# Optimization experiments

Measured on AMD Instinct MI355X. Metric: run time of the kernel, lower is better.

Reference implementation:

```python
import jax, jax.numpy as jnp
import numpy as np

N, C, HW, HEADS = 2048, 16, 8, 4
F = C * HW * HW  # 1024
E = 16384
EPS = 1e-5
NEG_SLOPE = 0.2


def _bn(x, g, b):
    # training-mode BatchNorm2d over (N, H, W)
    m = x.mean(axis=(0, 2, 3), keepdims=True)
    v = x.var(axis=(0, 2, 3), keepdims=True)
    return (x - m) * jax.lax.rsqrt(v + EPS) * g[None, :, None, None] + b[None, :, None, None]


def _conv1x1(x, w, b):
    # 1x1 conv == per-pixel linear: w is [out_c, in_c]
    return jnp.einsum('nchw,oc->nohw', x, w) + b[None, :, None, None]


def _gatv2(xf, edge_index, wl, bl, wr, br, att, bias_gat):
    # xf: [N, F] node features
    xl = (xf @ wl + bl).reshape(N, HEADS, F)  # source-side transform (lin_l)
    xr = (xf @ wr + br).reshape(N, HEADS, F)  # target-side transform (lin_r)
    src, dst = edge_index[0], edge_index[1]
    loops = jnp.arange(N)
    # PyG default: remove existing self loops (mask them) then add self loops
    src_f = jnp.concatenate([src, loops])
    dst_f = jnp.concatenate([dst, loops])
    valid = jnp.concatenate([src != dst, jnp.ones((N,), bool)])
    xj = xl[src_f]                                   # [E+N, HEADS, F] gather
    e = jax.nn.leaky_relu(xj + xr[dst_f], negative_slope=NEG_SLOPE)
    logits = jnp.einsum('ehf,hf->eh', e, att)        # [E+N, HEADS]
    logits = jnp.where(valid[:, None], logits, -jnp.inf)
    mx = jax.lax.stop_gradient(jax.ops.segment_max(logits, dst_f, num_segments=N))
    expv = jnp.where(valid[:, None], jnp.exp(logits - mx[dst_f]), 0.0)
    denom = jax.ops.segment_sum(expv, dst_f, num_segments=N)
    alpha = expv / denom[dst_f]                      # segment softmax over incoming edges
    out = jax.ops.segment_sum(alpha[:, :, None] * xj, dst_f, num_segments=N)  # [N, HEADS, F]
    return out.reshape(N, HEADS * F) + bias_gat


def setup_inputs() -> dict:
    key = jax.random.key(0)
    ks = jax.random.split(key, 8)
    s = 0.02
    return {
        'x': jax.random.normal(ks[0], (N, C, HW, HW), jnp.float32),
        'edge_index': jax.random.randint(ks[1], (2, E), 0, N),
        'w1': jax.random.normal(ks[2], (C, C), jnp.float32) * s,
        'b1': jnp.zeros((C,), jnp.float32),
        'g1': jnp.ones((C,), jnp.float32),
        'be1': jnp.zeros((C,), jnp.float32),
        'wl': jax.random.normal(ks[3], (F, HEADS * F), jnp.float32) * s,
        'bl': jnp.zeros((HEADS * F,), jnp.float32),
        'wr': jax.random.normal(ks[4], (F, HEADS * F), jnp.float32) * s,
        'br': jnp.zeros((HEADS * F,), jnp.float32),
        'att': jax.random.normal(ks[5], (HEADS, F), jnp.float32) * s,
        'bias_gat': jnp.zeros((HEADS * F,), jnp.float32),
        'w2': jax.random.normal(ks[6], (C, HEADS * C), jnp.float32) * s,
        'b2': jnp.zeros((C,), jnp.float32),
        'g2': jnp.ones((C,), jnp.float32),
        'be2': jnp.zeros((C,), jnp.float32),
    }


def reference(x, edge_index, w1, b1, g1, be1, wl, bl, wr, br, att, bias_gat, w2, b2, g2, be2):
    res = x
    y = _bn(_conv1x1(x, w1, b1), g1, be1)            # fc1: Conv2d 1x1 + BN
    yf = y.reshape(N, F)
    g = _gatv2(yf, edge_index, wl, bl, wr, br, att, bias_gat)
    g = g.reshape(N, HEADS * C, HW, HW)
    out = _bn(_conv1x1(g, w2, b2), g2, be2)          # fc2: Conv2d 1x1 + BN
    return out + res                                  # DropPath(0.0) == Identity
```

## Files before the change

kernel.cpp:

```cpp
#include <hip/hip_runtime.h>
#include <stdint.h>

#define N_NODES 2048
#define F_DIM   1024
#define HEADS   4
#define NF      4096
#define ROW     8192
#define E_EDGES 16384
#define MAXE    (E_EDGES + N_NODES)
#define BN_EPS  1e-5f
#define NSLOPE  0.2f

typedef unsigned short ushort_t;
typedef __attribute__((ext_vector_type(8))) short bf16x8;
typedef __attribute__((ext_vector_type(4))) float f32x4;
typedef __attribute__((ext_vector_type(8))) unsigned short us8;

__device__ __forceinline__ float b2f(unsigned short u) {
    union { unsigned int i; float f; } x; x.i = ((unsigned int)u) << 16; return x.f;
}
__device__ __forceinline__ unsigned short f2b(float f) {
    union { float f; unsigned int i; } x; x.f = f;
    unsigned int r = x.i + 0x7fffu + ((x.i >> 16) & 1u);
    return (unsigned short)(r >> 16);
}
__device__ __forceinline__ ushort_t ld_canon(const void* src, size_t i, int f32) {
    return f32 ? f2b(((const float*)src)[i]) : ((const ushort_t*)src)[i];
}
__device__ __forceinline__ float ld_f(const void* src, size_t i, int f32) {
    return f32 ? ((const float*)src)[i] : b2f(((const ushort_t*)src)[i]);
}

__global__ __launch_bounds__(1024) void k_csr(
    const int* __restrict__ ei_raw, const ushort_t* __restrict__ x_probe,
    int* __restrict__ offs, int* __restrict__ esrc, int* __restrict__ flags)
{
    __shared__ int cnt[2048];
    __shared__ int ts[1024];
    __shared__ int sflag;
    int t = threadIdx.x;
    if (t < 64) {
        int nz = (ei_raw[2 * t + 1] != 0) ? 1 : 0;
        unsigned long long m = __ballot(nz);
        if (t == 0) sflag = (m == 0ull) ? 1 : 0;
    } else if (t >= 64 && t < 96) {
        unsigned e = (x_probe[2 * (t - 64)] >> 7) & 0xFF;
        unsigned long long m = __ballot(e >= 0x90u);
        if (t == 64) flags[0] = (__popcll(m) >= 3) ? 1 : 0;
    }
    cnt[t] = 0; cnt[t + 1024] = 0;
    __syncthreads();
    int i64 = sflag;
    for (int idx = t; idx < MAXE; idx += 1024) {
        if (idx < E_EDGES) {
            int s = i64 ? ei_raw[2 * idx] : ei_raw[idx];
            int d = i64 ? ei_raw[2 * (E_EDGES + idx)] : ei_raw[E_EDGES + idx];
            if (s != d) atomicAdd(&cnt[d], 1);
        } else {
            atomicAdd(&cnt[idx - E_EDGES], 1);
        }
    }
    __syncthreads();
    int l0 = cnt[2 * t], l1 = cnt[2 * t + 1], tot = l0 + l1;
    ts[t] = tot;
    __syncthreads();
    for (int s = 1; s < 1024; s <<= 1) {
        int v = (t >= s) ? ts[t - s] : 0;
        __syncthreads();
        ts[t] += v;
        __syncthreads();
    }
    int run = ts[t] - tot;
    offs[2 * t] = run; offs[2 * t + 1] = run + l0;
    if (t == 1023) offs[2048] = ts[1023];
    __syncthreads();
    cnt[2 * t] = run; cnt[2 * t + 1] = run + l0;
    __syncthreads();
    for (int idx = t; idx < MAXE; idx += 1024) {
        if (idx < E_EDGES) {
            int s = i64 ? ei_raw[2 * idx] : ei_raw[idx];
            int d = i64 ? ei_raw[2 * (E_EDGES + idx)] : ei_raw[E_EDGES + idx];
            if (s != d) esrc[atomicAdd(&cnt[d], 1)] = s;
        } else {
            int n = idx - E_EDGES;
            esrc[atomicAdd(&cnt[n], 1)] = n;
        }
    }
}

__global__ __launch_bounds__(256) void k_fc1(
    const void* __restrict__ x, const void* __restrict__ w1, const void* __restrict__ b1,
    const int* __restrict__ flags,
    float* __restrict__ y0, float* __restrict__ ps, float* __restrict__ pq)
{
    __shared__ float xs[1024];
    __shared__ float sw[256];
    __shared__ float sb[16];
    int f32 = flags[0];
    int tid = threadIdx.x;
    sw[tid] = ld_f(w1, tid, f32);
    if (tid < 16) sb[tid] = ld_f(b1, tid, f32);
    int wave = tid >> 6, lane = tid & 63;
    float s[4] = {0,0,0,0}, q[4] = {0,0,0,0};
    for (int nn = 0; nn < 8; ++nn) {
        int n = blockIdx.x * 8 + nn;
        __syncthreads();
        #pragma unroll
        for (int i = 0; i < 4; ++i) {
            int idx = tid + i * 256;
            xs[idx] = ld_f(x, (size_t)n * 1024 + idx, f32);
        }
        __syncthreads();
        #pragma unroll
        for (int i = 0; i < 4; ++i) {
            int o = wave * 4 + i;
            float acc = sb[o];
            #pragma unroll
            for (int c = 0; c < 16; ++c) acc += xs[c * 64 + lane] * sw[o * 16 + c];
            y0[(size_t)n * 1024 + o * 64 + lane] = acc;
            s[i] += acc; q[i] += acc * acc;
        }
    }
    #pragma unroll
    for (int i = 0; i < 4; ++i)
        for (int mm = 1; mm < 64; mm <<= 1) {
            s[i] += __shfl_xor(s[i], mm);
            q[i] += __shfl_xor(q[i], mm);
        }
    if (lane == 0)
        #pragma unroll
        for (int i = 0; i < 4; ++i) {
            ps[blockIdx.x * 16 + wave * 4 + i] = s[i];
            pq[blockIdx.x * 16 + wave * 4 + i] = q[i];
        }
}

__global__ __launch_bounds__(256) void k_norm(
    const float* __restrict__ y0, const float* __restrict__ ps, const float* __restrict__ pq,
    const void* __restrict__ g1, const void* __restrict__ be1, const int* __restrict__ flags,
    ushort_t* __restrict__ xf)
{
    __shared__ float red[2][64];
    __shared__ float scs[16], shs[16];
    int f32 = flags[0];
    int t = threadIdx.x, lane = t & 63, wv = t >> 6;
    float s = 0.f, q = 0.f;
    #pragma unroll
    for (int i = 0; i < 16; ++i) { s += ps[i * 256 + t]; q += pq[i * 256 + t]; }
    s += __shfl_xor(s, 16); q += __shfl_xor(q, 16);
    s += __shfl_xor(s, 32); q += __shfl_xor(q, 32);
    if (lane < 16) { red[0][wv * 16 + lane] = s; red[1][wv * 16 + lane] = q; }
    __syncthreads();
    if (t < 16) {
        float S = red[0][t] + red[0][16 + t] + red[0][32 + t] + red[0][48 + t];
        float Q = red[1][t] + red[1][16 + t] + red[1][32 + t] + red[1][48 + t];
        const float inv = 1.0f / 131072.0f;
        float mean = S * inv;
        float var  = Q * inv - mean * mean;
        float sc = ld_f(g1, t, f32) * rsqrtf(var + BN_EPS);
        scs[t] = sc;
        shs[t] = ld_f(be1, t, f32) - mean * sc;
    }
    __syncthreads();
    int base = blockIdx.x * 4096;
    #pragma unroll
    for (int i = 0; i < 16; ++i) {
        int k = base + t + i * 256;
        int ch = (k >> 6) & 15;
        xf[k] = f2b(y0[k] * scs[ch] + shs[ch]);
    }
}

__global__ __launch_bounds__(256) void k_convT(
    const void* __restrict__ wl, const void* __restrict__ wr,
    const int* __restrict__ flags, ushort_t* __restrict__ wT)
{
    __shared__ ushort_t tl[64][65];
    int f32 = flags[0];
    const void* in = blockIdx.z ? wr : wl;
    ushort_t* outT = wT + (size_t)blockIdx.z * 4194304ull;
    int bx = blockIdx.x * 64, by = blockIdx.y * 64;
    #pragma unroll
    for (int i = 0; i < 16; ++i) {
        int idx = threadIdx.x + i * 256;
        int r = idx >> 6, c = idx & 63;
        tl[r][c] = ld_canon(in, (size_t)(by + r) * 4096 + bx + c, f32);
    }
    __syncthreads();
    #pragma unroll
    for (int i = 0; i < 16; ++i) {
        int idx = threadIdx.x + i * 256;
        int r = idx >> 6, c = idx & 63;
        outT[(size_t)(bx + r) * 1024 + by + c] = tl[c][r];
    }
}

__global__ __launch_bounds__(256) void k_gemm(
    const ushort_t* __restrict__ A, const ushort_t* __restrict__ BT,
    const void* __restrict__ blr, const void* __restrict__ brr,
    const int* __restrict__ flags, ushort_t* __restrict__ out)
{
    __shared__ __align__(16) ushort_t smem[16384];
    ushort_t* As0 = smem;
    ushort_t* As1 = smem + 4096;
    ushort_t* Bs0 = smem + 8192;
    ushort_t* Bs1 = smem + 12288;
    ushort_t* cs  = smem;
    int f32 = flags[0];
    int tid = threadIdx.x;
    int wv = tid >> 6, ln = tid & 63;
    int m0 = blockIdx.y * 128, n0 = blockIdx.x * 128;
    int wm = (wv >> 1) * 64, wn = (wv & 1) * 64;
    int lr = ln & 15, quad = ln >> 4;

    f32x4 acc[4][4];
    #pragma unroll
    for (int i = 0; i < 4; ++i)
        #pragma unroll
        for (int j = 0; j < 4; ++j) acc[i][j] = (f32x4){0.f, 0.f, 0.f, 0.f};

    for (int k0 = 0; k0 < 1024; k0 += 64) {
        #pragma unroll
        for (int i = 0; i < 2; ++i) {
            int cbase = i * 256 + wv * 64;
            int ci = cbase + ln;
            int m = ci >> 2, kc = ci & 3;
            const ushort_t* ga = A + (size_t)(m0 + m) * 1024 + k0 + kc * 8;
            __builtin_amdgcn_global_load_lds(
                (const __attribute__((address_space(1))) void*)ga,
                (__attribute__((address_space(3))) void*)(&As0[cbase * 8]), 16, 0, 0);
            __builtin_amdgcn_global_load_lds(
                (const __attribute__((address_space(1))) void*)(ga + 32),
                (__attribute__((address_space(3))) void*)(&As1[cbase * 8]), 16, 0, 0);
            const ushort_t* gb = BT + (size_t)(n0 + m) * 1024 + k0 + kc * 8;
            __builtin_amdgcn_global_load_lds(
                (const __attribute__((address_space(1))) void*)gb,
                (__attribute__((address_space(3))) void*)(&Bs0[cbase * 8]), 16, 0, 0);
            __builtin_amdgcn_global_load_lds(
                (const __attribute__((address_space(1))) void*)(gb + 32),
                (__attribute__((address_space(3))) void*)(&Bs1[cbase * 8]), 16, 0, 0);
        }
        __syncthreads();
        #pragma unroll
        for (int p = 0; p < 2; ++p) {
            const ushort_t* Ap = p ? As1 : As0;
            const ushort_t* Bp = p ? Bs1 : Bs0;
            bf16x8 af[4], bfr[4];
            #pragma unroll
            for (int i = 0; i < 4; ++i)
                af[i] = *(const bf16x8*)(&Ap[(wm + i * 16 + lr) * 32 + quad * 8]);
            #pragma unroll
            for (int j = 0; j < 4; ++j)
                bfr[j] = *(const bf16x8*)(&Bp[(wn + j * 16 + lr) * 32 + quad * 8]);
            #pragma unroll
            for (int i = 0; i < 4; ++i)
                #pragma unroll
                for (int j = 0; j < 4; ++j)
                    acc[i][j] = __builtin_amdgcn_mfma_f32_16x16x32_bf16(af[i], bfr[j], acc[i][j], 0, 0, 0);
        }
        __syncthreads();
    }
    float bj[4];
    #pragma unroll
    for (int j = 0; j < 4; ++j) {
        int colg = n0 + wn + j * 16 + lr;
        bj[j] = (colg < 4096) ? ld_f(blr, colg, f32) : ld_f(brr, colg - 4096, f32);
    }
    #pragma unroll
    for (int ph = 0; ph < 2; ++ph) {
        if ((wv >> 1) == ph) {
            #pragma unroll
            for (int i = 0; i < 4; ++i)
                #pragma unroll
                for (int j = 0; j < 4; ++j) {
                    int col = wn + j * 16 + lr;
                    #pragma unroll
                    for (int r = 0; r < 4; ++r)
                        cs[(i * 16 + quad * 4 + r) * 136 + col] = f2b(acc[i][j][r] + bj[j]);
                }
        }
        __syncthreads();
        #pragma unroll
        for (int rr = 0; rr < 4; ++rr) {
            int slot = rr * 256 + tid;
            int row = slot >> 4, seg = slot & 15;
            us8 v = *(const us8*)&cs[row * 136 + seg * 8];
            *(us8*)(out + (size_t)(m0 + ph * 64 + row) * ROW + n0 + seg * 8) = v;
        }
        __syncthreads();
    }
}

__global__ __launch_bounds__(256) void k_gat(
    const ushort_t* __restrict__ xlr,
    const void* __restrict__ att, const void* __restrict__ bg,
    const void* __restrict__ w2, const void* __restrict__ b2,
    const int* __restrict__ flags,
    const int* __restrict__ offsets, const int* __restrict__ esrc,
    float* __restrict__ z, float* __restrict__ ps2, float* __restrict__ pq2)
{
    __shared__ ushort_t gsb[4096];
    __shared__ float sw2[1024];
    __shared__ float sb2[16];
    int f32 = flags[0];
    int d = blockIdx.x;
    int tid = threadIdx.x;
    int h = tid >> 6, l = tid & 63;
    #pragma unroll
    for (int i = 0; i < 4; ++i) sw2[tid + i * 256] = ld_f(w2, tid + i * 256, f32);
    if (tid < 16) sb2[tid] = ld_f(b2, tid, f32);
    int off = offsets[d], deg = offsets[d + 1] - off;
    size_t hF = (size_t)h * F_DIM + l * 16;

    float xrv[16], attv[16];
    {
        const ushort_t* xp = xlr + ((size_t)d * ROW + NF + hF);
        us8 x0 = *(const us8*)xp, x1 = *(const us8*)(xp + 8);
        #pragma unroll
        for (int j = 0; j < 8; ++j) {
            xrv[j] = b2f(x0[j]); xrv[8 + j] = b2f(x1[j]);
            attv[j]     = ld_f(att, hF + j, f32);
            attv[8 + j] = ld_f(att, hF + 8 + j, f32);
        }
    }
    float acc[16];
    #pragma unroll
    for (int j = 0; j < 16; ++j) acc[j] = 0.f;
    float s_run = 0.f;

    for (int c0 = 0; c0 < deg; c0 += 64) {
        int cnt = min(64, deg - c0);
        int eidx = esrc[off + c0 + (l < cnt ? l : 0)];
        int e = 0;
        for (; e + 3 < cnt; e += 4) {
            int i0 = __shfl(eidx, e),     i1 = __shfl(eidx, e + 1);
            int i2 = __shfl(eidx, e + 2), i3 = __shfl(eidx, e + 3);
            const ushort_t* p0 = xlr + ((size_t)i0 * ROW + hF);
            const ushort_t* p1 = xlr + ((size_t)i1 * ROW + hF);
            const ushort_t* p2 = xlr + ((size_t)i2 * ROW + hF);
            const ushort_t* p3 = xlr + ((size_t)i3 * ROW + hF);
            us8 v0[4], v1[4];
            v0[0] = *(const us8*)p0; v1[0] = *(const us8*)(p0 + 8);
            v0[1] = *(const us8*)p1; v1[1] = *(const us8*)(p1 + 8);
            v0[2] = *(const us8*)p2; v1[2] = *(const us8*)(p2 + 8);
            v0[3] = *(const us8*)p3; v1[3] = *(const us8*)(p3 + 8);
            float tt[4];
            #pragma unroll
            for (int k = 0; k < 4; ++k) {
                float t0 = 0.f;
                #pragma unroll
                for (int j = 0; j < 8; ++j) {
                    float u;
                    u = b2f(v0[k][j]) + xrv[j];     u = u > 0.f ? u : NSLOPE * u; t0 += u * attv[j];
                    u = b2f(v1[k][j]) + xrv[8 + j]; u = u > 0.f ? u : NSLOPE * u; t0 += u * attv[8 + j];
                }
                tt[k] = t0;
            }
            #pragma unroll
            for (int mm = 1; mm < 64; mm <<= 1) {
                tt[0] += __shfl_xor(tt[0], mm);
                tt[1] += __shfl_xor(tt[1], mm);
                tt[2] += __shfl_xor(tt[2], mm);
                tt[3] += __shfl_xor(tt[3], mm);
            }
            float w0 = __expf(tt[0]), w1 = __expf(tt[1]);
            float w2v = __expf(tt[2]), w3 = __expf(tt[3]);
            s_run += w0 + w1 + w2v + w3;
            #pragma unroll
            for (int j = 0; j < 8; ++j) {
                acc[j]     += w0 * b2f(v0[0][j]) + w1 * b2f(v0[1][j])
                            + w2v * b2f(v0[2][j]) + w3 * b2f(v0[3][j]);
                acc[8 + j] += w0 * b2f(v1[0][j]) + w1 * b2f(v1[1][j])
                            + w2v * b2f(v1[2][j]) + w3 * b2f(v1[3][j]);
            }
        }
        for (; e < cnt; ++e) {
            int i0 = __shfl(eidx, e);
            const ushort_t* p = xlr + ((size_t)i0 * ROW + hF);
            us8 a0 = *(const us8*)p, a1 = *(const us8*)(p + 8);
            float t0 = 0.f;
            #pragma unroll
            for (int j = 0; j < 8; ++j) {
                float u;
                u = b2f(a0[j]) + xrv[j];     u = u > 0.f ? u : NSLOPE * u; t0 += u * attv[j];
                u = b2f(a1[j]) + xrv[8 + j]; u = u > 0.f ? u : NSLOPE * u; t0 += u * attv[8 + j];
            }
            #pragma unroll
            for (int mm = 1; mm < 64; mm <<= 1) t0 += __shfl_xor(t0, mm);
            float w0 = __expf(t0);
            s_run += w0;
            #pragma unroll
            for (int j = 0; j < 8; ++j) {
                acc[j]     += w0 * b2f(a0[j]);
                acc[8 + j] += w0 * b2f(a1[j]);
            }
        }
    }
    float inv = 1.0f / s_run;
    #pragma unroll
    for (int j = 0; j < 16; ++j)
        gsb[h * 1024 + l * 16 + j] = f2b(acc[j] * inv + ld_f(bg, hF + j, f32));
    __syncthreads();

    float s[4], q[4];
    #pragma unroll
    for (int i = 0; i < 4; ++i) {
        int o = h * 4 + i;
        float zv = sb2[o];
        #pragma unroll
        for (int k = 0; k < 64; ++k) zv += b2f(gsb[k * 64 + l]) * sw2[o * 64 + k];
        z[(size_t)d * 1024 + o * 64 + l] = zv;
        s[i] = zv; q[i] = zv * zv;
    }
    #pragma unroll
    for (int i = 0; i < 4; ++i)
        for (int mm = 1; mm < 64; mm <<= 1) {
            s[i] += __shfl_xor(s[i], mm);
            q[i] += __shfl_xor(q[i], mm);
        }
    if (l == 0)
        #pragma unroll
        for (int i = 0; i < 4; ++i) {
            ps2[d * 16 + h * 4 + i] = s[i];
            pq2[d * 16 + h * 4 + i] = q[i];
        }
}

__global__ __launch_bounds__(256) void k_bnf2(
    const float* __restrict__ ps, const float* __restrict__ pq,
    const void* __restrict__ g2, const void* __restrict__ be2,
    const int* __restrict__ flags, float* __restrict__ scale, float* __restrict__ shift)
{
    __shared__ float rs[16][16], rq[16][16];
    int f32 = flags[0];
    int t = threadIdx.x;
    int ch = t & 15, seg = t >> 4;
    float s = 0.f, q = 0.f;
    for (int j = 0; j < 128; ++j) {
        int b = seg * 128 + j;
        s += ps[b * 16 + ch]; q += pq[b * 16 + ch];
    }
    rs[seg][ch] = s; rq[seg][ch] = q;
    __syncthreads();
    if (t < 16) {
        float S = 0.f, Q = 0.f;
        #pragma unroll
        for (int g = 0; g < 16; ++g) { S += rs[g][t]; Q += rq[g][t]; }
        const float inv = 1.0f / 131072.0f;
        float mean = S * inv;
        float var  = Q * inv - mean * mean;
        float sc = ld_f(g2, t, f32) * rsqrtf(var + BN_EPS);
        scale[t] = sc;
        shift[t] = ld_f(be2, t, f32) - mean * sc;
    }
}

__global__ __launch_bounds__(256) void k_out(
    const float* __restrict__ z, const void* __restrict__ x,
    const float* __restrict__ scale, const float* __restrict__ shift,
    const int* __restrict__ flags, void* __restrict__ out)
{
    __shared__ float scs[16], shs[16];
    int f32 = flags[0];
    int t = threadIdx.x;
    if (t < 16) { scs[t] = scale[t]; shs[t] = shift[t]; }
    __syncthreads();
    size_t base = (size_t)blockIdx.x * 8192;
    #pragma unroll
    for (int i = 0; i < 32; ++i) {
        size_t k = base + t + i * 256;
        int ch = ((int)k >> 6) & 15;
        float val = z[k] * scs[ch] + shs[ch] + ld_f(x, k, f32);
        if (f32) ((float*)out)[k] = val;
        else     ((ushort_t*)out)[k] = f2b(val);
    }
}

extern "C" void kernel_launch(void* const* d_in, const int* in_sizes, int n_in,
                              void* d_out, int out_size, void* d_ws, size_t ws_size,
                              hipStream_t stream)
{
    const void* x   = d_in[0];
    const void* ei  = d_in[1];
    const void* w1  = d_in[2];
    const void* b1  = d_in[3];
    const void* g1  = d_in[4];
    const void* be1 = d_in[5];
    const void* wl  = d_in[6];
    const void* bl  = d_in[7];
    const void* wr  = d_in[8];
    const void* br  = d_in[9];
    const void* att = d_in[10];
    const void* bg  = d_in[11];
    const void* w2  = d_in[12];
    const void* b2  = d_in[13];
    const void* g2  = d_in[14];
    const void* be2 = d_in[15];
    (void)in_sizes; (void)n_in; (void)out_size; (void)ws_size;

    char* wsb = (char*)d_ws;
    size_t o = 0;
    auto alloc = [&](size_t bytes) -> void* {
        void* p = wsb + o;
        o = (o + bytes + 255) & ~(size_t)255;
        return p;
    };
    int*      flags = (int*)alloc(256);
    float*    y0    = (float*)alloc(2097152ull * 4);
    float*    z     = y0;
    ushort_t* xf    = (ushort_t*)alloc(2097152ull * 2);
    ushort_t* wT    = (ushort_t*)alloc(8388608ull * 2);
    ushort_t* xlr   = (ushort_t*)alloc(16777216ull * 2);
    float* p1s = (float*)alloc(256 * 16 * 4);
    float* p1q = (float*)alloc(256 * 16 * 4);
    float* p2s = (float*)alloc(2048 * 16 * 4);
    float* p2q = (float*)alloc(2048 * 16 * 4);
    float* ss  = (float*)alloc(64 * 4);
    int* offs  = (int*)alloc(2049 * 4);
    int* esrc  = (int*)alloc(MAXE * 4);

    k_csr<<<1, 1024, 0, stream>>>((const int*)ei, (const ushort_t*)x, offs, esrc, flags);
    k_fc1<<<256, 256, 0, stream>>>(x, w1, b1, flags, y0, p1s, p1q);
    k_norm<<<512, 256, 0, stream>>>(y0, p1s, p1q, g1, be1, flags, xf);
    k_convT<<<dim3(64, 16, 2), 256, 0, stream>>>(wl, wr, flags, wT);
    k_gemm<<<dim3(64, 16), 256, 0, stream>>>(xf, wT, bl, br, flags, xlr);
    k_gat<<<N_NODES, 256, 0, stream>>>(xlr, att, bg, w2, b2, flags, offs, esrc, z, p2s, p2q);
    k_bnf2<<<1, 256, 0, stream>>>(p2s, p2q, g2, be2, flags, ss, ss + 16);
    k_out<<<256, 256, 0, stream>>>(z, x, ss, ss + 16, flags, d_out);
}
```

Before: 297.5 us.

## Split GAT aggregation per head and move fc2 conv into separate kernel

```diff
diff --git a/kernel.cpp b/kernel.cpp
--- a/kernel.cpp
+++ b/kernel.cpp
@@ -291,24 +291,17 @@
     }
 }
 
-__global__ __launch_bounds__(256) void k_gat(
+__global__ __launch_bounds__(64) void k_gat(
     const ushort_t* __restrict__ xlr,
     const void* __restrict__ att, const void* __restrict__ bg,
-    const void* __restrict__ w2, const void* __restrict__ b2,
     const int* __restrict__ flags,
     const int* __restrict__ offsets, const int* __restrict__ esrc,
-    float* __restrict__ z, float* __restrict__ ps2, float* __restrict__ pq2)
-{
-    __shared__ ushort_t gsb[4096];
-    __shared__ float sw2[1024];
-    __shared__ float sb2[16];
-    int f32 = flags[0];
-    int d = blockIdx.x;
-    int tid = threadIdx.x;
-    int h = tid >> 6, l = tid & 63;
-    #pragma unroll
-    for (int i = 0; i < 4; ++i) sw2[tid + i * 256] = ld_f(w2, tid + i * 256, f32);
-    if (tid < 16) sb2[tid] = ld_f(b2, tid, f32);
+    ushort_t* __restrict__ g)
+{
+    int bx = blockIdx.x;
+    int d = bx >> 2, h = bx & 3;
+    int l = threadIdx.x;
+    int f32 = flags[0];
     int off = offsets[d], deg = offsets[d + 1] - off;
     size_t hF = (size_t)h * F_DIM + l * 16;
 
@@ -397,20 +390,54 @@
         }
     }
     float inv = 1.0f / s_run;
-    #pragma unroll
-    for (int j = 0; j < 16; ++j)
-        gsb[h * 1024 + l * 16 + j] = f2b(acc[j] * inv + ld_f(bg, hF + j, f32));
-    __syncthreads();
-
-    float s[4], q[4];
-    #pragma unroll
-    for (int i = 0; i < 4; ++i) {
-        int o = h * 4 + i;
-        float zv = sb2[o];
-        #pragma unroll
-        for (int k = 0; k < 64; ++k) zv += b2f(gsb[k * 64 + l]) * sw2[o * 64 + k];
-        z[(size_t)d * 1024 + o * 64 + l] = zv;
-        s[i] = zv; q[i] = zv * zv;
+    ushort_t* gp = g + ((size_t)d * NF + hF);
+    us8 outv0, outv1;
+    #pragma unroll
+    for (int j = 0; j < 8; ++j) {
+        outv0[j] = f2b(acc[j] * inv + ld_f(bg, hF + j, f32));
+        outv1[j] = f2b(acc[8 + j] * inv + ld_f(bg, hF + 8 + j, f32));
+    }
+    *(us8*)gp = outv0;
+    *(us8*)(gp + 8) = outv1;
+}
+
+__global__ __launch_bounds__(256) void k_fc2(
+    const ushort_t* __restrict__ g, const void* __restrict__ w2, const void* __restrict__ b2,
+    const int* __restrict__ flags,
+    float* __restrict__ z, float* __restrict__ ps, float* __restrict__ pq)
+{
+    __shared__ float gs[4096];
+    __shared__ float sw[1024];
+    __shared__ float sb[16];
+    int f32 = flags[0];
+    int tid = threadIdx.x;
+    #pragma unroll
+    for (int i = 0; i < 4; ++i) sw[tid + i * 256] = ld_f(w2, tid + i * 256, f32);
+    if (tid < 16) sb[tid] = ld_f(b2, tid, f32);
+    int wave = tid >> 6, lane = tid & 63;
+    float s[4] = {0,0,0,0}, q[4] = {0,0,0,0};
+    for (int nn = 0; nn < 8; ++nn) {
+        int n = blockIdx.x * 8 + nn;
+        __syncthreads();
+        {
+            const ushort_t* gp = g + (size_t)n * 4096 + tid * 16;
+            us8 v0 = *(const us8*)gp, v1 = *(const us8*)(gp + 8);
+            #pragma unroll
+            for (int j = 0; j < 8; ++j) {
+                gs[tid * 16 + j] = b2f(v0[j]);
+                gs[tid * 16 + 8 + j] = b2f(v1[j]);
+            }
+        }
+        __syncthreads();
+        #pragma unroll
+        for (int i = 0; i < 4; ++i) {
+            int o = wave * 4 + i;
+            float acc = sb[o];
+            #pragma unroll
+            for (int k = 0; k < 64; ++k) acc += gs[k * 64 + lane] * sw[o * 64 + k];
+            z[(size_t)n * 1024 + o * 64 + lane] = acc;
+            s[i] += acc; q[i] += acc * acc;
+        }
     }
     #pragma unroll
     for (int i = 0; i < 4; ++i)
@@ -418,52 +445,41 @@
             s[i] += __shfl_xor(s[i], mm);
             q[i] += __shfl_xor(q[i], mm);
         }
-    if (l == 0)
+    if (lane == 0)
         #pragma unroll
         for (int i = 0; i < 4; ++i) {
-            ps2[d * 16 + h * 4 + i] = s[i];
-            pq2[d * 16 + h * 4 + i] = q[i];
-        }
-}
-
-__global__ __launch_bounds__(256) void k_bnf2(
+            ps[blockIdx.x * 16 + wave * 4 + i] = s[i];
+            pq[blockIdx.x * 16 + wave * 4 + i] = q[i];
+        }
+}
+
+__global__ __launch_bounds__(256) void k_out(
+    const float* __restrict__ z, const void* __restrict__ x,
     const float* __restrict__ ps, const float* __restrict__ pq,
     const void* __restrict__ g2, const void* __restrict__ be2,
-    const int* __restrict__ flags, float* __restrict__ scale, float* __restrict__ shift)
-{
-    __shared__ float rs[16][16], rq[16][16];
-    int f32 = flags[0];
-    int t = threadIdx.x;
-    int ch = t & 15, seg = t >> 4;
+    const int* __restrict__ flags, void* __restrict__ out)
+{
+    __shared__ float red[2][64];
+    __shared__ float scs[16], shs[16];
+    int f32 = flags[0];
+    int t = threadIdx.x, lane = t & 63, wv = t >> 6;
     float s = 0.f, q = 0.f;
-    for (int j = 0; j < 128; ++j) {
-        int b = seg * 128 + j;
-        s += ps[b * 16 + ch]; q += pq[b * 16 + ch];
-    }
-    rs[seg][ch] = s; rq[seg][ch] = q;
+    #pragma unroll
+    for (int i = 0; i < 16; ++i) { s += ps[i * 256 + t]; q += pq[i * 256 + t]; }
+    s += __shfl_xor(s, 16); q += __shfl_xor(q, 16);
+    s += __shfl_xor(s, 32); q += __shfl_xor(q, 32);
+    if (lane < 16) { red[0][wv * 16 + lane] = s; red[1][wv * 16 + lane] = q; }
     __syncthreads();
     if (t < 16) {
-        float S = 0.f, Q = 0.f;
-        #pragma unroll
-        for (int g = 0; g < 16; ++g) { S += rs[g][t]; Q += rq[g][t]; }
+        float S = red[0][t] + red[0][16 + t] + red[0][32 + t] + red[0][48 + t];
+        float Q = red[1][t] + red[1][16 + t] + red[1][32 + t] + red[1][48 + t];
         const float inv = 1.0f / 131072.0f;
         float mean = S * inv;
         float var  = Q * inv - mean * mean;
         float sc = ld_f(g2, t, f32) * rsqrtf(var + BN_EPS);
-        scale[t] = sc;
-        shift[t] = ld_f(be2, t, f32) - mean * sc;
-    }
-}
-
-__global__ __launch_bounds__(256) void k_out(
-    const float* __restrict__ z, const void* __restrict__ x,
-    const float* __restrict__ scale, const float* __restrict__ shift,
-    const int* __restrict__ flags, void* __restrict__ out)
-{
-    __shared__ float scs[16], shs[16];
-    int f32 = flags[0];
-    int t = threadIdx.x;
-    if (t < 16) { scs[t] = scale[t]; shs[t] = shift[t]; }
+        scs[t] = sc;
+        shs[t] = ld_f(be2, t, f32) - mean * sc;
+    }
     __syncthreads();
     size_t base = (size_t)blockIdx.x * 8192;
     #pragma unroll
@@ -510,12 +526,12 @@
     float*    z     = y0;
     ushort_t* xf    = (ushort_t*)alloc(2097152ull * 2);
     ushort_t* wT    = (ushort_t*)alloc(8388608ull * 2);
+    ushort_t* gbuf  = wT;
     ushort_t* xlr   = (ushort_t*)alloc(16777216ull * 2);
     float* p1s = (float*)alloc(256 * 16 * 4);
     float* p1q = (float*)alloc(256 * 16 * 4);
-    float* p2s = (float*)alloc(2048 * 16 * 4);
-    float* p2q = (float*)alloc(2048 * 16 * 4);
-    float* ss  = (float*)alloc(64 * 4);
+    float* p2s = (float*)alloc(256 * 16 * 4);
+    float* p2q = (float*)alloc(256 * 16 * 4);
     int* offs  = (int*)alloc(2049 * 4);
     int* esrc  = (int*)alloc(MAXE * 4);
 
@@ -524,7 +540,7 @@
     k_norm<<<512, 256, 0, stream>>>(y0, p1s, p1q, g1, be1, flags, xf);
     k_convT<<<dim3(64, 16, 2), 256, 0, stream>>>(wl, wr, flags, wT);
     k_gemm<<<dim3(64, 16), 256, 0, stream>>>(xf, wT, bl, br, flags, xlr);
-    k_gat<<<N_NODES, 256, 0, stream>>>(xlr, att, bg, w2, b2, flags, offs, esrc, z, p2s, p2q);
-    k_bnf2<<<1, 256, 0, stream>>>(p2s, p2q, g2, be2, flags, ss, ss + 16);
-    k_out<<<256, 256, 0, stream>>>(z, x, ss, ss + 16, flags, d_out);
-}
+    k_gat<<<N_NODES * HEADS, 64, 0, stream>>>(xlr, att, bg, flags, offs, esrc, gbuf);
+    k_fc2<<<256, 256, 0, stream>>>(gbuf, w2, b2, flags, z, p2s, p2q);
+    k_out<<<256, 256, 0, stream>>>(z, x, p2s, p2q, g2, be2, flags, d_out);
+}
```

Result: faster. 286.6 us (-3.7%).
